# Kernel tuning notes

Hardware: AMD Instinct MI355X
Metric: run time of the kernel (lower is better)

## Reference

```python
import jax, jax.numpy as jnp
import numpy as np

D_MODEL = 512
NHEAD = 8
D_K = D_MODEL // NHEAD
SCALE = float(np.sqrt(D_K))


def setup_inputs() -> dict:
    key = jax.random.key(0)
    ks = jax.random.split(key, 11)
    B, S = 2, 4096
    std = 1.0 / np.sqrt(D_MODEL)
    inp = {
        'q': jax.random.normal(ks[0], (B, S, D_MODEL), jnp.float32),
        'k': jax.random.normal(ks[1], (B, S, D_MODEL), jnp.float32),
        'v': jax.random.normal(ks[2], (B, S, D_MODEL), jnp.float32),
        'w_q': jax.random.normal(ks[3], (D_MODEL, D_MODEL), jnp.float32) * std,
        'b_q': jax.random.normal(ks[4], (D_MODEL,), jnp.float32) * std,
        'w_k': jax.random.normal(ks[5], (D_MODEL, D_MODEL), jnp.float32) * std,
        'b_k': jax.random.normal(ks[6], (D_MODEL,), jnp.float32) * std,
        'w_v': jax.random.normal(ks[7], (D_MODEL, D_MODEL), jnp.float32) * std,
        'b_v': jax.random.normal(ks[8], (D_MODEL,), jnp.float32) * std,
        'w_o': jax.random.normal(ks[9], (D_MODEL, D_MODEL), jnp.float32) * std,
        'b_o': jax.random.normal(ks[10], (D_MODEL,), jnp.float32) * std,
    }
    return inp


def reference(q, k, v, w_q, b_q, w_k, b_k, w_v, b_v, w_o, b_o):
    B, S, _ = q.shape
    # torch Linear: y = x @ W.T + b
    def proj(x, W, b):
        y = x @ W.T + b
        return y.reshape(B, -1, NHEAD, D_K).transpose(0, 2, 1, 3)  # [B,H,S,Dk]
    qh = proj(q, w_q, b_q)
    kh = proj(k, w_k, b_k)
    vh = proj(v, w_v, b_v)
    scores = jnp.einsum('bhsd,bhtd->bhst', qh, kh) / SCALE  # [B,H,S,S]
    attn = jax.nn.softmax(scores, axis=-1)
    out = jnp.einsum('bhst,bhtd->bhsd', attn, vh)  # [B,H,S,Dk]
    out = out.transpose(0, 2, 1, 3).reshape(B, S, D_MODEL)
    return out @ w_o.T + b_o
```

## Files before the change

kernel.cpp:

```cpp
#include <hip/hip_runtime.h>
#include <stdint.h>

#define DM 512
#define S_LEN 4096
#define NH 8
#define DK 64

typedef __attribute__((ext_vector_type(8))) short bf16x8;
typedef __attribute__((ext_vector_type(4))) float f32x4;

#define QSCALE 0.18033688011112042f
#define NEGBIAS -17.312340490667562f

__device__ inline ushort f2bf(float f) {
  union { float f; uint32_t u; } v; v.f = f;
  uint32_t r = v.u + 0x7fff + ((v.u >> 16) & 1);
  return (ushort)(r >> 16);
}
__device__ inline uint32_t fu(float f) {
  union { float f; uint32_t u; } v; v.f = f; return v.u;
}
__device__ inline uint32_t pktrunc(float lo, float hi) {
  return __builtin_amdgcn_perm(fu(hi), fu(lo), 0x07060302);
}

__device__ inline void async_cp16(const void* g, void* l) {
  __builtin_amdgcn_global_load_lds((const __attribute__((address_space(1))) void*)g,
                                   (__attribute__((address_space(3))) void*)l, 16, 0, 0);
}

__global__ __launch_bounds__(256) void cvt_w(const float4* __restrict__ s0, ushort* __restrict__ d0,
                                             const float4* __restrict__ s1, ushort* __restrict__ d1,
                                             const float4* __restrict__ s2, ushort* __restrict__ d2,
                                             const float4* __restrict__ s3, ushort* __restrict__ d3) {
  int i = blockIdx.x * 256 + threadIdx.x;
  { float4 v = s0[i]; ushort4 o = {f2bf(v.x), f2bf(v.y), f2bf(v.z), f2bf(v.w)}; *(ushort4*)&d0[i * 4] = o; }
  { float4 v = s1[i]; ushort4 o = {f2bf(v.x), f2bf(v.y), f2bf(v.z), f2bf(v.w)}; *(ushort4*)&d1[i * 4] = o; }
  { float4 v = s2[i]; ushort4 o = {f2bf(v.x), f2bf(v.y), f2bf(v.z), f2bf(v.w)}; *(ushort4*)&d2[i * 4] = o; }
  { float4 v = s3[i]; ushort4 o = {f2bf(v.x), f2bf(v.y), f2bf(v.z), f2bf(v.w)}; *(ushort4*)&d3[i * 4] = o; }
}

__global__ __launch_bounds__(256) void gemm_proj(
    const float* __restrict__ q, const float* __restrict__ k, const float* __restrict__ v,
    const ushort* __restrict__ wq, const ushort* __restrict__ wk, const ushort* __restrict__ wv,
    const float* __restrict__ bq, const float* __restrict__ bk, const float* __restrict__ bv,
    ushort* __restrict__ Qh, ushort* __restrict__ Kh, ushort* __restrict__ VhT) {
  const float* A; const ushort* Bt; const float* bias; float cs;
  if (blockIdx.z == 0)      { A = q; Bt = wq; bias = bq; cs = QSCALE; }
  else if (blockIdx.z == 1) { A = k; Bt = wk; bias = bk; cs = 1.0f; }
  else                      { A = v; Bt = wv; bias = bv; cs = 1.0f; }

  __shared__ float  Asf[2][2048];
  __shared__ ushort Bsp[2][4096];
  const int tid = threadIdx.x;
  const int w = tid >> 6, lane = tid & 63;
  const int quad = lane >> 4, l16 = lane & 15;
  const int wm = w >> 1, wn = w & 1;
  const int m0 = blockIdx.x * 64, n0 = blockIdx.y * 128;
  const f32x4 zero4 = {0.f, 0.f, 0.f, 0.f};

  f32x4 acc[2][4];
  #pragma unroll
  for (int i = 0; i < 2; i++)
    #pragma unroll
    for (int j = 0; j < 4; j++) acc[i][j] = zero4;

  #define PSTAGE(KB, BUF) do {                                                        \
    const int k0_ = (KB) * 32;                                                        \
    _Pragma("unroll")                                                                 \
    for (int r_ = 0; r_ < 2; r_++) {                       \
      int idx = r_ * 256 + tid;                                                       \
      int c = idx >> 6, row = idx & 63;                                               \
      async_cp16(&A[(size_t)(m0 + row) * DM + k0_ + c * 4], &Asf[BUF][idx * 4]);      \
    }                                                                                 \
    _Pragma("unroll")                                                                 \
    for (int r_ = 0; r_ < 2; r_++) {                       \
      int idx = r_ * 256 + tid;                                                       \
      int c = idx >> 7, row = idx & 127;                                              \
      async_cp16(&Bt[(size_t)(n0 + row) * DM + k0_ + c * 8], &Bsp[BUF][idx * 8]);     \
    }                                                                                 \
  } while (0)

  PSTAGE(0, 0);
  __syncthreads();

  for (int kb = 0; kb < 16; kb++) {
    const int cur = kb & 1;
    if (kb < 15) PSTAGE(kb + 1, cur ^ 1);
    bf16x8 af[2], bfr[4];
    #pragma unroll
    for (int i = 0; i < 2; i++) {
      int r = wm * 32 + i * 16 + l16;
      f32x4 a0 = *(const f32x4*)&Asf[cur][((quad * 2 + 0) * 64 + r) * 4];
      f32x4 a1 = *(const f32x4*)&Asf[cur][((quad * 2 + 1) * 64 + r) * 4];
      union { bf16x8 v; uint32_t u[4]; } t;
      t.u[0] = pktrunc(a0.x, a0.y); t.u[1] = pktrunc(a0.z, a0.w);
      t.u[2] = pktrunc(a1.x, a1.y); t.u[3] = pktrunc(a1.z, a1.w);
      af[i] = t.v;
    }
    #pragma unroll
    for (int j = 0; j < 4; j++)
      bfr[j] = *(const bf16x8*)&Bsp[cur][(quad * 128 + wn * 64 + j * 16 + l16) * 8];
    #pragma unroll
    for (int i = 0; i < 2; i++)
      #pragma unroll
      for (int j = 0; j < 4; j++)
        acc[i][j] = __builtin_amdgcn_mfma_f32_16x16x32_bf16(af[i], bfr[j], acc[i][j], 0, 0, 0);
    __syncthreads();
  }

  if (blockIdx.z != 2) {
    ushort* C = (blockIdx.z == 0) ? Qh : Kh;
    #pragma unroll
    for (int j = 0; j < 4; j++) {
      int col_g = n0 + wn * 64 + j * 16 + l16;
      float bv = bias[col_g];
      int h = col_g >> 6, d = col_g & 63;
      #pragma unroll
      for (int i = 0; i < 2; i++) {
        #pragma unroll
        for (int r = 0; r < 4; r++) {
          int row_g = m0 + wm * 32 + i * 16 + quad * 4 + r;
          int b = row_g >> 12, s = row_g & 4095;
          C[(((size_t)(b * NH + h) << 12) + s) * DK + d] = f2bf((acc[i][j][r] + bv) * cs);
        }
      }
    }
  } else {
    #pragma unroll
    for (int j = 0; j < 4; j++) {
      int col_g = n0 + wn * 64 + j * 16 + l16;
      float bv = bias[col_g];
      int h = col_g >> 6, d = col_g & 63;
      #pragma unroll
      for (int i = 0; i < 2; i++) {
        int row0 = m0 + wm * 32 + i * 16 + quad * 4;
        int b = row0 >> 12, s0 = row0 & 4095;
        int sl = s0 & 31;
        int sp = (s0 & ~31) | (((sl >> 2) & 3) << 3) | (((sl >> 4) & 1) << 2);
        ushort4 pk = {f2bf(acc[i][j][0] + bv), f2bf(acc[i][j][1] + bv),
                      f2bf(acc[i][j][2] + bv), f2bf(acc[i][j][3] + bv)};
        *(ushort4*)&VhT[((size_t)(b * NH + h) * DK + d) * S_LEN + sp] = pk;
      }
    }
  }
}

__global__ __launch_bounds__(256) void gemm_out(const ushort* __restrict__ A,
                                                const ushort* __restrict__ Bt,
                                                const float* __restrict__ bias,
                                                float* __restrict__ C) {
  __shared__ ushort Asp[2][2048];
  __shared__ ushort Bsp[2][4096];
  const int tid = threadIdx.x;
  const int w = tid >> 6, lane = tid & 63;
  const int quad = lane >> 4, l16 = lane & 15;
  const int wm = w >> 1, wn = w & 1;
  const int m0 = blockIdx.x * 64, n0 = blockIdx.y * 128;
  const f32x4 zero4 = {0.f, 0.f, 0.f, 0.f};

  f32x4 acc[2][4];
  #pragma unroll
  for (int i = 0; i < 2; i++)
    #pragma unroll
    for (int j = 0; j < 4; j++) acc[i][j] = zero4;

  #define OSTAGE(KB, BUF) do {                                                        \
    const int k0_ = (KB) * 32;                                                        \
    { int idx = tid;                                                \
      int c = idx >> 6, row = idx & 63;                                               \
      async_cp16(&A[(size_t)(m0 + row) * DM + k0_ + c * 8], &Asp[BUF][idx * 8]); }    \
    _Pragma("unroll")                                                                 \
    for (int r_ = 0; r_ < 2; r_++) {                                \
      int idx = r_ * 256 + tid;                                                       \
      int c = idx >> 7, row = idx & 127;                                              \
      async_cp16(&Bt[(size_t)(n0 + row) * DM + k0_ + c * 8], &Bsp[BUF][idx * 8]);     \
    }                                                                                 \
  } while (0)

  OSTAGE(0, 0);
  __syncthreads();

  for (int kb = 0; kb < 16; kb++) {
    const int cur = kb & 1;
    if (kb < 15) OSTAGE(kb + 1, cur ^ 1);
    bf16x8 af[2], bfr[4];
    #pragma unroll
    for (int i = 0; i < 2; i++)
      af[i]  = *(const bf16x8*)&Asp[cur][(quad * 64 + wm * 32 + i * 16 + l16) * 8];
    #pragma unroll
    for (int j = 0; j < 4; j++)
      bfr[j] = *(const bf16x8*)&Bsp[cur][(quad * 128 + wn * 64 + j * 16 + l16) * 8];
    #pragma unroll
    for (int i = 0; i < 2; i++)
      #pragma unroll
      for (int j = 0; j < 4; j++)
        acc[i][j] = __builtin_amdgcn_mfma_f32_16x16x32_bf16(af[i], bfr[j], acc[i][j], 0, 0, 0);
    __syncthreads();
  }

  #pragma unroll
  for (int j = 0; j < 4; j++) {
    int col_g = n0 + wn * 64 + j * 16 + l16;
    float bv = bias[col_g];
    #pragma unroll
    for (int i = 0; i < 2; i++) {
      #pragma unroll
      for (int r = 0; r < 4; r++) {
        int row_g = m0 + wm * 32 + i * 16 + quad * 4 + r;
        C[(size_t)row_g * DM + col_g] = acc[i][j][r] + bv;
      }
    }
  }
}

typedef union { bf16x8 v; uint32_t u[4]; } pfu;

__global__ __launch_bounds__(512, 4) void attn(const ushort* __restrict__ Qh,
                                               const ushort* __restrict__ Kh,
                                               const ushort* __restrict__ VhT,
                                               ushort* __restrict__ O) {
  __shared__ ushort smem[2][16384];
  const int tid = threadIdx.x;
  const int w = tid >> 6, lane = tid & 63;
  const int quad = lane >> 4, l16 = lane & 15;
  const int half = w >> 2;
  const int qw = w & 3;
  const int bh = blockIdx.x;
  const int q0 = blockIdx.y * 128 + qw * 32;
  const size_t base = (size_t)bh * S_LEN * DK;
  const f32x4 zero4 = {0.f, 0.f, 0.f, 0.f};
  const f32x4 negb = {NEGBIAS, NEGBIAS, NEGBIAS, NEGBIAS};
  const short one_bf = (short)0x3F80;
  const bf16x8 ones = {one_bf, one_bf, one_bf, one_bf, one_bf, one_bf, one_bf, one_bf};

  if (blockIdx.y >= 16) {
    #pragma unroll
    for (int i = 0; i < 6; i++) __builtin_amdgcn_s_sleep(7);
  }

  bf16x8 qf[2][2];
  #pragma unroll
  for (int i = 0; i < 2; i++)
    #pragma unroll
    for (int c = 0; c < 2; c++)
      qf[i][c] = *(const bf16x8*)&Qh[base + (size_t)(q0 + i * 16 + l16) * DK + c * 32 + quad * 8];

  f32x4 o[2][4];
  f32x4 l_acc[2];
  #pragma unroll
  for (int i = 0; i < 2; i++) {
    l_acc[i] = zero4;
    #pragma unroll
    for (int n = 0; n < 4; n++) o[i][n] = zero4;
  }

  #define STAGE(IT, BUF) do {                                                         \
    const int t0_ = (IT) * 128;                                                       \
    _Pragma("unroll")                                                                 \
    for (int r_ = 0; r_ < 2; r_++) {                                                  \
      int idx = r_ * 512 + tid;                                                       \
      int row = idx >> 3;                                                             \
      int cl = ((idx & 7) << 4) ^ ((row & 7) << 4);                                   \
      async_cp16(&Kh[base + (size_t)(t0_ + row) * DK + (cl >> 1)], &smem[BUF][idx * 8]); \
    }                                                                                 \
    _Pragma("unroll")                                                                 \
    for (int r_ = 0; r_ < 2; r_++) {                                                  \
      int idx = r_ * 512 + tid;                                                       \
      int row = idx >> 4;                                                             \
      int cl = ((idx & 15) << 4) ^ ((row & 7) << 4);                                  \
      async_cp16(&VhT[base + (size_t)row * S_LEN + t0_ + (cl >> 1)], &smem[BUF][8192 + idx * 8]); \
    }                                                                                 \
  } while (0)

  STAGE(0, 0);
  __syncthreads();

  const int swz = (l16 & 7) << 4;

  for (int it = 0; it < 32; it++) {
    const int cur = it & 1;
    if (it < 31) STAGE(it + 1, cur ^ 1);
    const ushort* Kb = &smem[cur][0];
    const ushort* Vb = &smem[cur][8192];

    bf16x8 kf[4][2];
    #pragma unroll
    for (int s = 0; s < 4; s++) {
      int row = half * 64 + s * 16 + l16;
      kf[s][0] = *(const bf16x8*)&Kb[row * 64 + ((( 0 + quad * 16) ^ swz) >> 1)];
      kf[s][1] = *(const bf16x8*)&Kb[row * 64 + (((64 + quad * 16) ^ swz) >> 1)];
    }
    f32x4 sc[2][4];
    __builtin_amdgcn_s_setprio(1);
    #pragma unroll
    for (int i = 0; i < 2; i++)
      #pragma unroll
      for (int s = 0; s < 4; s++) {
        f32x4 t = negb;
        t = __builtin_amdgcn_mfma_f32_16x16x32_bf16(kf[s][0], qf[i][0], t, 0, 0, 0);
        t = __builtin_amdgcn_mfma_f32_16x16x32_bf16(kf[s][1], qf[i][1], t, 0, 0, 0);
        sc[i][s] = t;
      }
    __builtin_amdgcn_s_setprio(0);
    float p[2][4][4];
    #pragma unroll
    for (int i = 0; i < 2; i++)
      #pragma unroll
      for (int s = 0; s < 4; s++)
        #pragma unroll
        for (int r = 0; r < 4; r++)
          p[i][s][r] = __builtin_amdgcn_exp2f(sc[i][s][r]);
    pfu pf[2][2];
    #pragma unroll
    for (int i = 0; i < 2; i++)
      #pragma unroll
      for (int ppl = 0; ppl < 2; ppl++) {
        int s0 = ppl * 2, s1 = ppl * 2 + 1;
        pf[i][ppl].u[0] = pktrunc(p[i][s0][0], p[i][s0][1]);
        pf[i][ppl].u[1] = pktrunc(p[i][s0][2], p[i][s0][3]);
        pf[i][ppl].u[2] = pktrunc(p[i][s1][0], p[i][s1][1]);
        pf[i][ppl].u[3] = pktrunc(p[i][s1][2], p[i][s1][3]);
        l_acc[i] = __builtin_amdgcn_mfma_f32_16x16x32_bf16(pf[i][ppl].v, ones, l_acc[i], 0, 0, 0);
      }
    bf16x8 vf[4][2];
    #pragma unroll
    for (int n = 0; n < 4; n++) {
      int row = n * 16 + l16;
      #pragma unroll
      for (int ppl = 0; ppl < 2; ppl++)
        vf[n][ppl] = *(const bf16x8*)&Vb[row * 128 + ((((half * 2 + ppl) * 64 + quad * 16) ^ swz) >> 1)];
    }
    __builtin_amdgcn_s_setprio(1);
    #pragma unroll
    for (int n = 0; n < 4; n++)
      #pragma unroll
      for (int ppl = 0; ppl < 2; ppl++)
        #pragma unroll
        for (int i = 0; i < 2; i++)
          o[i][n] = __builtin_amdgcn_mfma_f32_16x16x32_bf16(pf[i][ppl].v, vf[n][ppl], o[i][n], 0, 0, 0);
    __builtin_amdgcn_s_setprio(0);

    __syncthreads();
  }

  float* red = (float*)smem;
  const int roff = (qw * 64 + lane) * 40;
  if (half == 1) {
    #pragma unroll
    for (int i = 0; i < 2; i++) {
      #pragma unroll
      for (int n = 0; n < 4; n++)
        *(f32x4*)&red[roff + (i * 4 + n) * 4] = o[i][n];
      *(f32x4*)&red[roff + 32 + i * 4] = l_acc[i];
    }
  }
  __syncthreads();
  if (half == 0) {
    #pragma unroll
    for (int i = 0; i < 2; i++) {
      #pragma unroll
      for (int n = 0; n < 4; n++)
        o[i][n] += *(const f32x4*)&red[roff + (i * 4 + n) * 4];
      l_acc[i] += *(const f32x4*)&red[roff + 32 + i * 4];
    }
    const int b = bh >> 3, h = bh & 7;
    #pragma unroll
    for (int i = 0; i < 2; i++) {
      #pragma unroll
      for (int r = 0; r < 4; r++) {
        float inv = 1.0f / l_acc[i][r];
        int qq = q0 + i * 16 + quad * 4 + r;
        #pragma unroll
        for (int n = 0; n < 4; n++) {
          int d = n * 16 + l16;
          O[(size_t)(b * S_LEN + qq) * DM + h * DK + d] = f2bf(o[i][n][r] * inv);
        }
      }
    }
  }
}

extern "C" void kernel_launch(void* const* d_in, const int* in_sizes, int n_in,
                              void* d_out, int out_size, void* d_ws, size_t ws_size,
                              hipStream_t stream) {
  const float* q   = (const float*)d_in[0];
  const float* k   = (const float*)d_in[1];
  const float* v   = (const float*)d_in[2];
  const float* w_q = (const float*)d_in[3];
  const float* b_q = (const float*)d_in[4];
  const float* w_k = (const float*)d_in[5];
  const float* b_k = (const float*)d_in[6];
  const float* w_v = (const float*)d_in[7];
  const float* b_v = (const float*)d_in[8];
  const float* w_o = (const float*)d_in[9];
  const float* b_o = (const float*)d_in[10];

  const size_t W_ELEMS = (size_t)DM * DM;
  const size_t HEADS_ELEMS = (size_t)2 * NH * S_LEN * DK;
  ushort* wqb = (ushort*)d_ws;
  ushort* wkb = wqb + W_ELEMS;
  ushort* wvb = wkb + W_ELEMS;
  ushort* wob = wvb + W_ELEMS;
  ushort* Qh  = wob + W_ELEMS;
  ushort* Kh  = Qh + HEADS_ELEMS;
  ushort* VhT = Kh + HEADS_ELEMS;
  ushort* AttO = VhT + HEADS_ELEMS;

  cvt_w<<<256, 256, 0, stream>>>((const float4*)w_q, wqb, (const float4*)w_k, wkb,
                                 (const float4*)w_v, wvb, (const float4*)w_o, wob);
  gemm_proj<<<dim3(128, 4, 3), 256, 0, stream>>>(q, k, v, wqb, wkb, wvb,
                                                 b_q, b_k, b_v, Qh, Kh, VhT);
  attn<<<dim3(16, 32), 512, 0, stream>>>(Qh, Kh, VhT, AttO);
  gemm_out<<<dim3(128, 4), 256, 0, stream>>>(AttO, wob, b_o, (float*)d_out);
}
```

Measured before the change: 245.4 us.

## Triple-buffer projection GEMM loads with vmcnt waits and one barrier per step

Both projection GEMMs move from double to triple-buffered LDS staging. Each k-step now waits on vmcnt for only the older stage's async copies and uses a single s_barrier, replacing the two __syncthreads per iteration, and the k-loop is fully unrolled. This lets the next stage's loads overlap the current stage's MFMAs with less synchronisation, at the cost of more LDS per block (possibly lower occupancy) and reliance on precise vmcnt counts.

After: 238.3 us. 2.9% less time.

```diff
diff --git a/kernel.cpp b/kernel.cpp
--- a/kernel.cpp
+++ b/kernel.cpp
@@ -50,8 +50,8 @@
   else if (blockIdx.z == 1) { A = k; Bt = wk; bias = bk; cs = 1.0f; }
   else                      { A = v; Bt = wv; bias = bv; cs = 1.0f; }
 
-  __shared__ float  Asf[2][2048];
-  __shared__ ushort Bsp[2][4096];
+  __shared__ float  Asf[3][2048];
+  __shared__ ushort Bsp[3][4096];
   const int tid = threadIdx.x;
   const int w = tid >> 6, lane = tid & 63;
   const int quad = lane >> 4, l16 = lane & 15;
@@ -67,26 +67,35 @@
 
   #define PSTAGE(KB, BUF) do {                                                        \
     const int k0_ = (KB) * 32;                                                        \
+    float*  asf_ = &Asf[BUF][0];                                                      \
+    ushort* bsp_ = &Bsp[BUF][0];                                                      \
     _Pragma("unroll")                                                                 \
     for (int r_ = 0; r_ < 2; r_++) {                       \
       int idx = r_ * 256 + tid;                                                       \
       int c = idx >> 6, row = idx & 63;                                               \
-      async_cp16(&A[(size_t)(m0 + row) * DM + k0_ + c * 4], &Asf[BUF][idx * 4]);      \
+      async_cp16(&A[(size_t)(m0 + row) * DM + k0_ + c * 4], &asf_[idx * 4]);          \
     }                                                                                 \
     _Pragma("unroll")                                                                 \
     for (int r_ = 0; r_ < 2; r_++) {                       \
       int idx = r_ * 256 + tid;                                                       \
       int c = idx >> 7, row = idx & 127;                                              \
-      async_cp16(&Bt[(size_t)(n0 + row) * DM + k0_ + c * 8], &Bsp[BUF][idx * 8]);     \
+      async_cp16(&Bt[(size_t)(n0 + row) * DM + k0_ + c * 8], &bsp_[idx * 8]);         \
     }                                                                                 \
   } while (0)
 
   PSTAGE(0, 0);
-  __syncthreads();
-
+
+  #pragma unroll
   for (int kb = 0; kb < 16; kb++) {
-    const int cur = kb & 1;
-    if (kb < 15) PSTAGE(kb + 1, cur ^ 1);
+    if (kb < 15) {
+      PSTAGE(kb + 1, (kb + 1) % 3);
+      asm volatile("s_waitcnt vmcnt(4)" ::: "memory");
+    } else {
+      asm volatile("s_waitcnt vmcnt(0)" ::: "memory");
+    }
+    __builtin_amdgcn_s_barrier();
+    __builtin_amdgcn_sched_barrier(0);
+    const int cur = kb % 3;
     bf16x8 af[2], bfr[4];
     #pragma unroll
     for (int i = 0; i < 2; i++) {
@@ -106,7 +115,6 @@
       #pragma unroll
       for (int j = 0; j < 4; j++)
         acc[i][j] = __builtin_amdgcn_mfma_f32_16x16x32_bf16(af[i], bfr[j], acc[i][j], 0, 0, 0);
-    __syncthreads();
   }
 
   if (blockIdx.z != 2) {
@@ -150,8 +158,8 @@
                                                 const ushort* __restrict__ Bt,
                                                 const float* __restrict__ bias,
                                                 float* __restrict__ C) {
-  __shared__ ushort Asp[2][2048];
-  __shared__ ushort Bsp[2][4096];
+  __shared__ ushort Asp[3][2048];
+  __shared__ ushort Bsp[3][4096];
   const int tid = threadIdx.x;
   const int w = tid >> 6, lane = tid & 63;
   const int quad = lane >> 4, l16 = lane & 15;
@@ -167,23 +175,32 @@
 
   #define OSTAGE(KB, BUF) do {                                                        \
     const int k0_ = (KB) * 32;                                                        \
+    ushort* asp_ = &Asp[BUF][0];                                                      \
+    ushort* bsp_ = &Bsp[BUF][0];                                                      \
     { int idx = tid;                                                \
       int c = idx >> 6, row = idx & 63;                                               \
-      async_cp16(&A[(size_t)(m0 + row) * DM + k0_ + c * 8], &Asp[BUF][idx * 8]); }    \
+      async_cp16(&A[(size_t)(m0 + row) * DM + k0_ + c * 8], &asp_[idx * 8]); }        \
     _Pragma("unroll")                                                                 \
     for (int r_ = 0; r_ < 2; r_++) {                                \
       int idx = r_ * 256 + tid;                                                       \
       int c = idx >> 7, row = idx & 127;                                              \
-      async_cp16(&Bt[(size_t)(n0 + row) * DM + k0_ + c * 8], &Bsp[BUF][idx * 8]);     \
+      async_cp16(&Bt[(size_t)(n0 + row) * DM + k0_ + c * 8], &bsp_[idx * 8]);         \
     }                                                                                 \
   } while (0)
 
   OSTAGE(0, 0);
-  __syncthreads();
-
+
+  #pragma unroll
   for (int kb = 0; kb < 16; kb++) {
-    const int cur = kb & 1;
-    if (kb < 15) OSTAGE(kb + 1, cur ^ 1);
+    if (kb < 15) {
+      OSTAGE(kb + 1, (kb + 1) % 3);
+      asm volatile("s_waitcnt vmcnt(3)" ::: "memory");
+    } else {
+      asm volatile("s_waitcnt vmcnt(0)" ::: "memory");
+    }
+    __builtin_amdgcn_s_barrier();
+    __builtin_amdgcn_sched_barrier(0);
+    const int cur = kb % 3;
     bf16x8 af[2], bfr[4];
     #pragma unroll
     for (int i = 0; i < 2; i++)
@@ -196,7 +213,6 @@
       #pragma unroll
       for (int j = 0; j < 4; j++)
         acc[i][j] = __builtin_amdgcn_mfma_f32_16x16x32_bf16(af[i], bfr[j], acc[i][j], 0, 0, 0);
-    __syncthreads();
   }
 
   #pragma unroll
```
